# Kernel optimization log

Measured on AMD Instinct MI355X. Metric: run time of the kernel, lower is better.

The kernel has to match this reference:

```python
import jax, jax.numpy as jnp
import numpy as np

EPS = 1e-5

def _layernorm(x, g, b):
    m = jnp.mean(x, axis=-1, keepdims=True)
    v = jnp.mean(jnp.square(x - m), axis=-1, keepdims=True)
    return (x - m) * jax.lax.rsqrt(v + EPS) * g + b

def setup_inputs() -> dict:
    key = jax.random.key(0)
    ks = jax.random.split(key, 8)
    B, T, C, H, D = 4096, 16, 512, 8, 64
    s = 0.02
    return {
        "x": jax.random.normal(ks[0], (B, T, C), jnp.float32),
        "ln1_g": jnp.ones((C,), jnp.float32),
        "ln1_b": jnp.zeros((C,), jnp.float32),
        "wq": jax.random.normal(ks[1], (H, C, D), jnp.float32) * s,
        "wk": jax.random.normal(ks[2], (H, C, D), jnp.float32) * s,
        "wv": jax.random.normal(ks[3], (H, C, D), jnp.float32) * s,
        "w_proj": jax.random.normal(ks[4], (H * D, C), jnp.float32) * s,
        "b_proj": jnp.zeros((C,), jnp.float32),
        "ln2_g": jnp.ones((C,), jnp.float32),
        "ln2_b": jnp.zeros((C,), jnp.float32),
        "w1": jax.random.normal(ks[5], (C, 4 * C), jnp.float32) * s,
        "b1": jnp.zeros((4 * C,), jnp.float32),
        "w2": jax.random.normal(ks[6], (4 * C, C), jnp.float32) * s,
        "b2": jnp.zeros((C,), jnp.float32),
    }

def reference(x, ln1_g, ln1_b, wq, wk, wv, w_proj, b_proj, ln2_g, ln2_b, w1, b1, w2, b2):
    B, T, C = x.shape
    H, _, D = wq.shape
    h = _layernorm(x, ln1_g, ln1_b)
    # fused per-head projections (original looped over 8 Head modules)
    q = jnp.einsum('btc,hcd->bhtd', h, wq)
    k = jnp.einsum('btc,hcd->bhtd', h, wk)
    v = jnp.einsum('btc,hcd->bhtd', h, wv)
    logits = jnp.einsum('bhtd,bhsd->bhts', q, k) * (D ** -0.5)
    causal = jnp.tril(jnp.ones((T, T), bool))
    logits = jnp.where(causal, logits, -jnp.inf)
    att = jax.nn.softmax(logits, axis=-1)  # dropout is identity at eval
    o = jnp.einsum('bhts,bhsd->bhtd', att, v)
    o = o.transpose(0, 2, 1, 3).reshape(B, T, H * D)  # concat heads in order
    y = o @ w_proj + b_proj + x  # residual 1
    h2 = _layernorm(y, ln2_g, ln2_b)
    f = jax.nn.relu(h2 @ w1 + b1) @ w2 + b2
    return f + y  # residual 2
```

## Files before the change

### kernel.cpp

```cpp
#include <hip/hip_runtime.h>
#include <hip/hip_bf16.h>

typedef __attribute__((ext_vector_type(8))) short s16x8;
typedef __attribute__((ext_vector_type(4))) short s16x4;
typedef __attribute__((ext_vector_type(4))) float f32x4;

#define GAS __attribute__((address_space(1)))
#define LAS __attribute__((address_space(3)))

#define WAITV(N) asm volatile("s_waitcnt vmcnt(" #N ")" ::: "memory")
#define WAITL() asm volatile("s_waitcnt lgkmcnt(0)" ::: "memory")
#define BAR() __builtin_amdgcn_s_barrier()

__device__ __forceinline__ float b2f(unsigned short u) {
  union { unsigned int i; float f; } x; x.i = ((unsigned int)u) << 16; return x.f;
}
__device__ __forceinline__ unsigned short f2b(float f) {
  union { float f; unsigned int i; } x; x.f = f;
  unsigned int r = x.i + 0x7fffu + ((x.i >> 16) & 1u);
  return (unsigned short)(r >> 16);
}

__device__ __forceinline__ void gl16(const unsigned short* g, unsigned short* l) {
  __builtin_amdgcn_global_load_lds((const GAS unsigned int*)g,
                                   (LAS unsigned int*)l, 16, 0, 0);
}

__global__ __launch_bounds__(256) void pack_x_k(const float* __restrict__ x,
                                                unsigned short* __restrict__ xb) {
  size_t i = ((size_t)blockIdx.x * 256 + threadIdx.x) * 8;
  f32x4 a = *(const f32x4*)(x + i);
  f32x4 b = *(const f32x4*)(x + i + 4);
  float vals[8] = {a.x, a.y, a.z, a.w, b.x, b.y, b.z, b.w};
  s16x8 o;
#pragma unroll
  for (int k = 0; k < 8; k++) o[k] = (short)f2b(vals[k]);
  *(s16x8*)(xb + i) = o;
}

__global__ __launch_bounds__(256) void pack_qkv_k(const float* __restrict__ wq,
                                                  const float* __restrict__ wk,
                                                  const float* __restrict__ wv,
                                                  unsigned short* __restrict__ dst) {
  int idx = blockIdx.x * 256 + threadIdx.x;
  int n = idx >> 9, c = idx & 511;
  int sel = n >> 9;
  int hn = n & 511;
  const float* src = sel == 0 ? wq : (sel == 1 ? wk : wv);
  float v = src[((hn >> 6) << 15) + (c << 6) + (hn & 63)];
  dst[idx] = f2b(v);
}

__global__ __launch_bounds__(256) void pack_T_k(const float* __restrict__ src,
                                                unsigned short* __restrict__ dst,
                                                int K, int N) {
  int idx = blockIdx.x * 256 + threadIdx.x;
  int n = idx / K, k = idx % K;
  dst[idx] = f2b(src[(long long)k * N + n]);
}

__global__ __launch_bounds__(256) void ln_k(const float* __restrict__ in,
                                            const float* __restrict__ g,
                                            const float* __restrict__ bb,
                                            unsigned short* __restrict__ out) {
  int row = blockIdx.x * 4 + (threadIdx.x >> 6);
  int lane = threadIdx.x & 63;
  const float* p = in + (size_t)row * 512 + lane * 8;
  f32x4 a = *(const f32x4*)p;
  f32x4 b = *(const f32x4*)(p + 4);
  float vals[8] = {a.x, a.y, a.z, a.w, b.x, b.y, b.z, b.w};
  float s = 0.f, q = 0.f;
#pragma unroll
  for (int i = 0; i < 8; i++) { s += vals[i]; q += vals[i] * vals[i]; }
#pragma unroll
  for (int off = 1; off < 64; off <<= 1) {
    s += __shfl_xor(s, off);
    q += __shfl_xor(q, off);
  }
  float mean = s * (1.0f / 512.0f);
  float rstd = rsqrtf(q * (1.0f / 512.0f) - mean * mean + 1e-5f);
  const float* gp = g + lane * 8;
  const float* bp = bb + lane * 8;
  s16x8 o;
#pragma unroll
  for (int i = 0; i < 8; i++) o[i] = (short)f2b((vals[i] - mean) * rstd * gp[i] + bp[i]);
  *(s16x8*)(out + (size_t)row * 512 + lane * 8) = o;
}

__global__ __launch_bounds__(256) void ln_b_k(const unsigned short* __restrict__ in,
                                              const float* __restrict__ g,
                                              const float* __restrict__ bb,
                                              unsigned short* __restrict__ out) {
  int row = blockIdx.x * 4 + (threadIdx.x >> 6);
  int lane = threadIdx.x & 63;
  s16x8 v8 = *(const s16x8*)(in + (size_t)row * 512 + lane * 8);
  float vals[8];
#pragma unroll
  for (int i = 0; i < 8; i++) vals[i] = b2f((unsigned short)v8[i]);
  float s = 0.f, q = 0.f;
#pragma unroll
  for (int i = 0; i < 8; i++) { s += vals[i]; q += vals[i] * vals[i]; }
#pragma unroll
  for (int off = 1; off < 64; off <<= 1) {
    s += __shfl_xor(s, off);
    q += __shfl_xor(q, off);
  }
  float mean = s * (1.0f / 512.0f);
  float rstd = rsqrtf(q * (1.0f / 512.0f) - mean * mean + 1e-5f);
  const float* gp = g + lane * 8;
  const float* bp = bb + lane * 8;
  s16x8 o;
#pragma unroll
  for (int i = 0; i < 8; i++) o[i] = (short)f2b((vals[i] - mean) * rstd * gp[i] + bp[i]);
  *(s16x8*)(out + (size_t)row * 512 + lane * 8) = o;
}

__global__ __launch_bounds__(256) void attn_k(const unsigned short* __restrict__ qkv,
                                              unsigned short* __restrict__ o) {
  int w = (blockIdx.x << 2) + (threadIdx.x >> 6);
  int lane = threadIdx.x & 63;
  int b = w >> 3, h = w & 7;
  int t = lane >> 2, p = lane & 3;

  size_t rowq = (size_t)(b * 16 + t) * 1536 + h * 64 + p * 16;
  float q[16];
  {
    s16x8 q0 = *(const s16x8*)(qkv + rowq);
    s16x8 q1 = *(const s16x8*)(qkv + rowq + 8);
#pragma unroll
    for (int i = 0; i < 8; i++) {
      q[i] = b2f((unsigned short)q0[i]) * 0.125f;
      q[8 + i] = b2f((unsigned short)q1[i]) * 0.125f;
    }
  }
  float lg[16];
  size_t kbase = (size_t)(b * 16) * 1536 + 512 + h * 64 + p * 16;
#pragma unroll
  for (int s = 0; s < 16; s++) {
    const unsigned short* kp = qkv + kbase + (size_t)s * 1536;
    s16x8 k0 = *(const s16x8*)kp;
    s16x8 k1 = *(const s16x8*)(kp + 8);
    float d = 0.f;
#pragma unroll
    for (int i = 0; i < 8; i++)
      d += q[i] * b2f((unsigned short)k0[i]) + q[8 + i] * b2f((unsigned short)k1[i]);
    d += __shfl_xor(d, 1);
    d += __shfl_xor(d, 2);
    lg[s] = d;
  }
  float mx = -1e30f;
#pragma unroll
  for (int s = 0; s < 16; s++)
    if (s <= t) mx = fmaxf(mx, lg[s]);
  float den = 0.f;
#pragma unroll
  for (int s = 0; s < 16; s++) {
    float e = (s <= t) ? __expf(lg[s] - mx) : 0.f;
    lg[s] = e;
    den += e;
  }
  float inv = 1.f / den;
  float acc[16] = {};
  size_t vbase = kbase + 512;
#pragma unroll
  for (int s = 0; s < 16; s++) {
    const unsigned short* vp = qkv + vbase + (size_t)s * 1536;
    s16x8 v0 = *(const s16x8*)vp;
    s16x8 v1 = *(const s16x8*)(vp + 8);
    float a = lg[s] * inv;
#pragma unroll
    for (int i = 0; i < 8; i++) {
      acc[i] += a * b2f((unsigned short)v0[i]);
      acc[8 + i] += a * b2f((unsigned short)v1[i]);
    }
  }
  size_t orow = (size_t)(b * 16 + t) * 512 + h * 64 + p * 16;
  s16x8 r0, r1;
#pragma unroll
  for (int i = 0; i < 8; i++) {
    r0[i] = (short)f2b(acc[i]);
    r1[i] = (short)f2b(acc[8 + i]);
  }
  *(s16x8*)(o + orow) = r0;
  *(s16x8*)(o + orow + 8) = r1;
}

enum { EPI_BF16 = 0, EPI_RESF32 = 1, EPI_RELU = 2, EPI_YBB = 3, EPI_OUTB = 4 };

template <int EPI>
__global__ __launch_bounds__(512) void gemm_bt(
    const unsigned short* __restrict__ A,
    const unsigned short* __restrict__ Bt,
    int K, int N, int nT,
    const float* __restrict__ bias, const void* __restrict__ res,
    float* __restrict__ outF, unsigned short* __restrict__ outB) {
  __shared__ __align__(16) unsigned char SM[131072];

  int tid = threadIdx.x;
  int lid = ((int)blockIdx.x & 7) * ((int)gridDim.x >> 3) + ((int)blockIdx.x >> 3);
  int mBase = (lid / nT) * 256;
  int nBase = (lid % nT) * 256;

  int lane = tid & 63;
  int wid = tid >> 6;
  int wm = wid >> 2;
  int wn = wid & 3;
  int l15 = lane & 15;
  int s4 = lane >> 4;
  int lr4 = s4 * 4;
  int fc = ((s4 ^ ((l15 >> 1) & 3)) << 3);

  int srow = tid >> 2;
  int scol = (((tid & 3) ^ ((srow >> 1) & 3)) << 3);
  const unsigned short* pa = A + (size_t)(mBase + srow) * K + scol;
  const unsigned short* pb = Bt + (size_t)(nBase + srow) * K + scol;
  size_t k128 = (size_t)128 * K;
  unsigned short* dstB = (unsigned short*)SM + wid * 512;

  f32x4 acc[8][4] = {};

  auto stgA = [&](int slot, int a, int t) {
    gl16(pa + (size_t)a * k128 + t * 32, dstB + slot * 4096);
  };
  auto stgB = [&](int slot, int b, int t) {
    gl16(pb + (size_t)b * k128 + t * 32, dstB + slot * 4096);
  };

  int NT = K >> 5;
  stgA(0, 0, 0);  stgA(1, 1, 0);
  stgB(2, 0, 0);  stgB(3, 1, 0);
  stgA(4, 0, 1);  stgA(5, 1, 1);
  stgB(6, 0, 1);  stgB(7, 1, 1);
  stgA(8, 0, 2);  stgA(9, 1, 2);

  for (int t = 0; t < NT; ++t) {
    int sb = (t & 3) << 2;
    const unsigned short* hA = (const unsigned short*)SM + (size_t)(sb + wm) * 4096;
    const unsigned short* hB = (const unsigned short*)SM + (size_t)(sb + 2 + (wn >> 1)) * 4096;
    int br = (wn & 1) * 64;
    s16x8 af[4], bf[4];

    if (t + 2 < NT) {
      int s2 = ((t + 2) & 3) << 2;
      stgB(s2 + 2, 0, t + 2);
      stgB(s2 + 3, 1, t + 2);
      WAITV(8);
    } else if (t == NT - 2) {
      WAITV(4);
    } else {
      WAITV(0);
    }
    BAR();
#pragma unroll
    for (int n = 0; n < 4; ++n)
      bf[n] = *(const s16x8*)&hB[(br + n * 16 + l15) * 32 + fc];
#pragma unroll
    for (int m = 0; m < 4; ++m)
      af[m] = *(const s16x8*)&hA[(m * 16 + l15) * 32 + fc];
    __builtin_amdgcn_s_setprio(1);
#pragma unroll
    for (int m = 0; m < 4; ++m)
#pragma unroll
      for (int n = 0; n < 4; ++n)
        acc[m][n] = __builtin_amdgcn_mfma_f32_16x16x32_bf16(af[m], bf[n], acc[m][n], 0, 0, 0);
    __builtin_amdgcn_s_setprio(0);

#pragma unroll
    for (int m = 0; m < 4; ++m)
      af[m] = *(const s16x8*)&hA[((m + 4) * 16 + l15) * 32 + fc];
    if (t + 3 < NT) {
      int s3 = ((t + 3) & 3) << 2;
      stgA(s3 + 0, 0, t + 3);
      stgA(s3 + 1, 1, t + 3);
    }
    BAR();
    __builtin_amdgcn_s_setprio(1);
#pragma unroll
    for (int m = 0; m < 4; ++m)
#pragma unroll
      for (int n = 0; n < 4; ++n)
        acc[m + 4][n] = __builtin_amdgcn_mfma_f32_16x16x32_bf16(af[m], bf[n], acc[m + 4][n], 0, 0, 0);
    __builtin_amdgcn_s_setprio(0);
  }
  BAR();

  if (EPI == EPI_RESF32 || EPI == EPI_OUTB) {
#pragma unroll
    for (int n = 0; n < 4; n++) {
      int gc2 = nBase + wn * 64 + n * 16 + l15;
      float bv = bias[gc2];
#pragma unroll
      for (int m = 0; m < 8; m++) {
#pragma unroll
        for (int j = 0; j < 4; j++) {
          int gr = mBase + wm * 128 + m * 16 + lr4 + j;
          size_t off = (size_t)gr * N + gc2;
          float v = acc[m][n][j] + bv;
          if (EPI == EPI_RESF32)
            outF[off] = v + ((const float*)res)[off];
          else
            outF[off] = v + b2f(((const unsigned short*)res)[off]);
        }
      }
    }
  } else {
    float* ep = (float*)SM + wid * 1088;
    int colc = nBase + wn * 64 + l15 * 4;
    f32x4 bias4 = {0.f, 0.f, 0.f, 0.f};
    if (EPI != EPI_BF16) bias4 = *(const f32x4*)&bias[colc];
#pragma unroll
    for (int m = 0; m < 8; m++) {
#pragma unroll
      for (int n = 0; n < 4; n++)
#pragma unroll
        for (int j = 0; j < 4; j++)
          ep[(lr4 + j) * 68 + n * 16 + l15] = acc[m][n][j];
      WAITL();
#pragma unroll
      for (int rd = 0; rd < 4; rd++) {
        int r = s4 + 4 * rd;
        f32x4 v = *(const f32x4*)&ep[r * 68 + l15 * 4];
        v.x += bias4.x; v.y += bias4.y; v.z += bias4.z; v.w += bias4.w;
        int gr = mBase + wm * 128 + m * 16 + r;
        size_t off = (size_t)gr * N + colc;
        if (EPI == EPI_YBB) {
          s16x4 rb = *(const s16x4*)((const unsigned short*)res + off);
          v.x += b2f((unsigned short)rb[0]); v.y += b2f((unsigned short)rb[1]);
          v.z += b2f((unsigned short)rb[2]); v.w += b2f((unsigned short)rb[3]);
        } else if (EPI == EPI_RELU) {
          v.x = fmaxf(v.x, 0.f); v.y = fmaxf(v.y, 0.f);
          v.z = fmaxf(v.z, 0.f); v.w = fmaxf(v.w, 0.f);
        }
        s16x4 o;
        o[0] = (short)f2b(v.x); o[1] = (short)f2b(v.y);
        o[2] = (short)f2b(v.z); o[3] = (short)f2b(v.w);
        *(s16x4*)(outB + off) = o;
      }
      WAITL();
    }
  }
}

extern "C" void kernel_launch(void* const* d_in, const int* in_sizes, int n_in,
                              void* d_out, int out_size, void* d_ws, size_t ws_size,
                              hipStream_t stream) {
  const float* x      = (const float*)d_in[0];
  const float* ln1_g  = (const float*)d_in[1];
  const float* ln1_b  = (const float*)d_in[2];
  const float* wq     = (const float*)d_in[3];
  const float* wk     = (const float*)d_in[4];
  const float* wv     = (const float*)d_in[5];
  const float* w_proj = (const float*)d_in[6];
  const float* b_proj = (const float*)d_in[7];
  const float* ln2_g  = (const float*)d_in[8];
  const float* ln2_b  = (const float*)d_in[9];
  const float* w1     = (const float*)d_in[10];
  const float* b1     = (const float*)d_in[11];
  const float* w2     = (const float*)d_in[12];
  const float* b2     = (const float*)d_in[13];
  float* out = (float*)d_out;

  char* ws = (char*)d_ws;
  unsigned short* qkvT  = (unsigned short*)(ws + 0);
  unsigned short* projT = (unsigned short*)(ws + 1572864);
  unsigned short* w1T   = (unsigned short*)(ws + 2097152);
  unsigned short* w2T   = (unsigned short*)(ws + 4194304);
  unsigned short* hbuf  = (unsigned short*)(ws + 6291456);
  unsigned short* qkv   = (unsigned short*)(ws + 73400320);
  unsigned short* xb    = (unsigned short*)(ws + 274726912);
  unsigned short* obuf  = (unsigned short*)(ws + 341835776);
  unsigned short* ybuf  = (unsigned short*)(ws + 408944640);
  bool yb16 = ws_size >= 476053504ull;

  pack_qkv_k<<<3072, 256, 0, stream>>>(wq, wk, wv, qkvT);
  pack_T_k<<<1024, 256, 0, stream>>>(w_proj, projT, 512, 512);
  pack_T_k<<<4096, 256, 0, stream>>>(w1, w1T, 512, 2048);
  pack_T_k<<<4096, 256, 0, stream>>>(w2, w2T, 2048, 512);

  unsigned short* ff = qkv;
  if (yb16) {
    pack_x_k<<<16384, 256, 0, stream>>>(x, xb);
    ln_b_k<<<16384, 256, 0, stream>>>(xb, ln1_g, ln1_b, hbuf);
    gemm_bt<EPI_BF16><<<1536, 512, 0, stream>>>(hbuf, qkvT, 512, 1536, 6,
                                                nullptr, nullptr, nullptr, qkv);
    attn_k<<<8192, 256, 0, stream>>>(qkv, obuf);
    gemm_bt<EPI_YBB><<<512, 512, 0, stream>>>(obuf, projT, 512, 512, 2,
                                              b_proj, xb, nullptr, ybuf);
    ln_b_k<<<16384, 256, 0, stream>>>(ybuf, ln2_g, ln2_b, hbuf);
    gemm_bt<EPI_RELU><<<2048, 512, 0, stream>>>(hbuf, w1T, 512, 2048, 8,
                                                b1, nullptr, nullptr, ff);
    gemm_bt<EPI_OUTB><<<512, 512, 0, stream>>>(ff, w2T, 2048, 512, 2,
                                               b2, ybuf, out, nullptr);
  } else {
    ln_k<<<16384, 256, 0, stream>>>(x, ln1_g, ln1_b, hbuf);
    gemm_bt<EPI_BF16><<<1536, 512, 0, stream>>>(hbuf, qkvT, 512, 1536, 6,
                                                nullptr, nullptr, nullptr, qkv);
    attn_k<<<8192, 256, 0, stream>>>(qkv, obuf);
    gemm_bt<EPI_RESF32><<<512, 512, 0, stream>>>(obuf, projT, 512, 512, 2,
                                                 b_proj, x, out, nullptr);
    ln_k<<<16384, 256, 0, stream>>>(out, ln2_g, ln2_b, hbuf);
    gemm_bt<EPI_RELU><<<2048, 512, 0, stream>>>(hbuf, w1T, 512, 2048, 8,
                                                b1, nullptr, nullptr, ff);
    gemm_bt<EPI_RESF32><<<512, 512, 0, stream>>>(ff, w2T, 2048, 512, 2,
                                                 b2, out, out, nullptr);
  }
}
```

Before: 760.0 us.

## Fuse x bf16 packing into LN1 and shrink GEMM to double-buffered LDS

LayerNorm 1 now reads the fp32 input once and writes both the bf16 copy of x (used later as the residual) and the normalized bf16 output. This removes a separate pack kernel and one full bf16 read of x. The GEMM drops from a 4-stage ring with 128KB of LDS to a 2-stage double buffer with 64KB, so two workgroups may fit per CU. The cost is less prefetch depth, so global-load latency may be harder to hide. LN1 now takes its statistics from the fp32 input rather than the bf16-rounded copy, which slightly changes the numerics.

```diff
diff --git a/kernel.cpp b/kernel.cpp
--- a/kernel.cpp
+++ b/kernel.cpp
@@ -24,18 +24,6 @@
 __device__ __forceinline__ void gl16(const unsigned short* g, unsigned short* l) {
   __builtin_amdgcn_global_load_lds((const GAS unsigned int*)g,
                                    (LAS unsigned int*)l, 16, 0, 0);
-}
-
-__global__ __launch_bounds__(256) void pack_x_k(const float* __restrict__ x,
-                                                unsigned short* __restrict__ xb) {
-  size_t i = ((size_t)blockIdx.x * 256 + threadIdx.x) * 8;
-  f32x4 a = *(const f32x4*)(x + i);
-  f32x4 b = *(const f32x4*)(x + i + 4);
-  float vals[8] = {a.x, a.y, a.z, a.w, b.x, b.y, b.z, b.w};
-  s16x8 o;
-#pragma unroll
-  for (int k = 0; k < 8; k++) o[k] = (short)f2b(vals[k]);
-  *(s16x8*)(xb + i) = o;
 }
 
 __global__ __launch_bounds__(256) void pack_qkv_k(const float* __restrict__ wq,
@@ -59,6 +47,39 @@
   dst[idx] = f2b(src[(long long)k * N + n]);
 }
 
+__global__ __launch_bounds__(256) void ln_fx_k(const float* __restrict__ in,
+                                               const float* __restrict__ g,
+                                               const float* __restrict__ bb,
+                                               unsigned short* __restrict__ out,
+                                               unsigned short* __restrict__ xb) {
+  int row = blockIdx.x * 4 + (threadIdx.x >> 6);
+  int lane = threadIdx.x & 63;
+  const float* p = in + (size_t)row * 512 + lane * 8;
+  f32x4 a = *(const f32x4*)p;
+  f32x4 b = *(const f32x4*)(p + 4);
+  float vals[8] = {a.x, a.y, a.z, a.w, b.x, b.y, b.z, b.w};
+  s16x8 xo;
+#pragma unroll
+  for (int i = 0; i < 8; i++) xo[i] = (short)f2b(vals[i]);
+  *(s16x8*)(xb + (size_t)row * 512 + lane * 8) = xo;
+  float s = 0.f, q = 0.f;
+#pragma unroll
+  for (int i = 0; i < 8; i++) { s += vals[i]; q += vals[i] * vals[i]; }
+#pragma unroll
+  for (int off = 1; off < 64; off <<= 1) {
+    s += __shfl_xor(s, off);
+    q += __shfl_xor(q, off);
+  }
+  float mean = s * (1.0f / 512.0f);
+  float rstd = rsqrtf(q * (1.0f / 512.0f) - mean * mean + 1e-5f);
+  const float* gp = g + lane * 8;
+  const float* bp = bb + lane * 8;
+  s16x8 o;
+#pragma unroll
+  for (int i = 0; i < 8; i++) o[i] = (short)f2b((vals[i] - mean) * rstd * gp[i] + bp[i]);
+  *(s16x8*)(out + (size_t)row * 512 + lane * 8) = o;
+}
+
 __global__ __launch_bounds__(256) void ln_k(const float* __restrict__ in,
                                             const float* __restrict__ g,
                                             const float* __restrict__ bb,
@@ -194,7 +215,7 @@
     int K, int N, int nT,
     const float* __restrict__ bias, const void* __restrict__ res,
     float* __restrict__ outF, unsigned short* __restrict__ outB) {
-  __shared__ __align__(16) unsigned char SM[131072];
+  __shared__ __align__(16) unsigned char SM[65536];
 
   int tid = threadIdx.x;
   int lid = ((int)blockIdx.x & 7) * ((int)gridDim.x >> 3) + ((int)blockIdx.x >> 3);
@@ -229,24 +250,19 @@
   int NT = K >> 5;
   stgA(0, 0, 0);  stgA(1, 1, 0);
   stgB(2, 0, 0);  stgB(3, 1, 0);
-  stgA(4, 0, 1);  stgA(5, 1, 1);
-  stgB(6, 0, 1);  stgB(7, 1, 1);
-  stgA(8, 0, 2);  stgA(9, 1, 2);
 
   for (int t = 0; t < NT; ++t) {
-    int sb = (t & 3) << 2;
+    int sb = (t & 1) << 2;
+    int sn = ((t + 1) & 1) << 2;
     const unsigned short* hA = (const unsigned short*)SM + (size_t)(sb + wm) * 4096;
     const unsigned short* hB = (const unsigned short*)SM + (size_t)(sb + 2 + (wn >> 1)) * 4096;
     int br = (wn & 1) * 64;
     s16x8 af[4], bf[4];
 
-    if (t + 2 < NT) {
-      int s2 = ((t + 2) & 3) << 2;
-      stgB(s2 + 2, 0, t + 2);
-      stgB(s2 + 3, 1, t + 2);
-      WAITV(8);
-    } else if (t == NT - 2) {
-      WAITV(4);
+    if (t + 1 < NT) {
+      stgA(sn + 0, 0, t + 1);
+      stgA(sn + 1, 1, t + 1);
+      WAITV(2);
     } else {
       WAITV(0);
     }
@@ -268,10 +284,9 @@
 #pragma unroll
     for (int m = 0; m < 4; ++m)
       af[m] = *(const s16x8*)&hA[((m + 4) * 16 + l15) * 32 + fc];
-    if (t + 3 < NT) {
-      int s3 = ((t + 3) & 3) << 2;
-      stgA(s3 + 0, 0, t + 3);
-      stgA(s3 + 1, 1, t + 3);
+    if (t + 1 < NT) {
+      stgB(sn + 2, 0, t + 1);
+      stgB(sn + 3, 1, t + 1);
     }
     BAR();
     __builtin_amdgcn_s_setprio(1);
@@ -379,8 +394,7 @@
 
   unsigned short* ff = qkv;
   if (yb16) {
-    pack_x_k<<<16384, 256, 0, stream>>>(x, xb);
-    ln_b_k<<<16384, 256, 0, stream>>>(xb, ln1_g, ln1_b, hbuf);
+    ln_fx_k<<<16384, 256, 0, stream>>>(x, ln1_g, ln1_b, hbuf, xb);
     gemm_bt<EPI_BF16><<<1536, 512, 0, stream>>>(hbuf, qkvT, 512, 1536, 6,
                                                 nullptr, nullptr, nullptr, qkv);
     attn_k<<<8192, 256, 0, stream>>>(qkv, obuf);
```

Measured after the change: 797.4 us. +4.9%, slower.
